# Kernel optimization log

Measured on AMD Instinct MI355X. Metric: run time of the kernel, lower is better.

The kernel has to match this reference:

```python
import jax, jax.numpy as jnp
import numpy as np

N_NODES = 50000
N_EDGES = 800000
D_IN = 128
D_OUT = 128
HEADS = 2
NEG_SLOPE = 0.2  # PyG GATConv default


def _gat_layer(x, src, dst, W, att_src, att_dst, bias):
    """One PyG-style GATConv with concat=False (mean over heads).
    x: [N, d_in], W: [d_in, H*d_out], att_src/att_dst: [H, d_out], bias: [d_out].
    Edge (j=src -> i=dst); softmax normalized over incoming edges of each dst node.
    """
    n = x.shape[0]
    d_out = att_src.shape[1]
    h = (x @ W).reshape(n, HEADS, d_out)                       # [N, H, D]
    a_s = jnp.einsum('nhd,hd->nh', h, att_src)                 # [N, H]
    a_d = jnp.einsum('nhd,hd->nh', h, att_dst)                 # [N, H]
    e = jax.nn.leaky_relu(a_s[src] + a_d[dst], NEG_SLOPE)      # [E, H]
    # numerically stable segment softmax over dst
    m = jax.ops.segment_max(e, dst, num_segments=n)            # [N, H]
    p = jnp.exp(e - m[dst])                                    # [E, H]
    s = jax.ops.segment_sum(p, dst, num_segments=n)            # [N, H]
    alpha = p / s[dst]                                         # [E, H]
    msg = h[src] * alpha[:, :, None]                           # [E, H, D]
    out = jax.ops.segment_sum(msg, dst, num_segments=n)        # [N, H, D]
    return out.mean(axis=1) + bias                             # concat=False -> mean heads


def setup_inputs() -> dict:
    key = jax.random.key(0)
    ks = jax.random.split(key, 10)
    sc = 0.05
    return {
        'x': jax.random.normal(ks[0], (N_NODES, D_IN), dtype=jnp.float32),
        'edge_index': jax.random.randint(ks[1], (2, N_EDGES), 0, N_NODES, dtype=jnp.int64),
        'W1': jax.random.normal(ks[2], (D_IN, HEADS * D_IN), dtype=jnp.float32) * sc,
        'att_src1': jax.random.normal(ks[3], (HEADS, D_IN), dtype=jnp.float32) * sc,
        'att_dst1': jax.random.normal(ks[4], (HEADS, D_IN), dtype=jnp.float32) * sc,
        'b1': jnp.zeros((D_IN,), dtype=jnp.float32),
        'W2': jax.random.normal(ks[5], (D_IN, HEADS * D_OUT), dtype=jnp.float32) * sc,
        'att_src2': jax.random.normal(ks[6], (HEADS, D_OUT), dtype=jnp.float32) * sc,
        'att_dst2': jax.random.normal(ks[7], (HEADS, D_OUT), dtype=jnp.float32) * sc,
        'b2': jnp.zeros((D_OUT,), dtype=jnp.float32),
    }


def reference(x, edge_index, W1, att_src1, att_dst1, b1, W2, att_src2, att_dst2, b2):
    n = x.shape[0]
    # PyG GATConv adds self-loops by default -> every node has >=1 incoming edge
    loops = jnp.arange(n, dtype=edge_index.dtype)
    src = jnp.concatenate([edge_index[0], loops])
    dst = jnp.concatenate([edge_index[1], loops])
    x = _gat_layer(x, src, dst, W1, att_src1, att_dst1, b1)
    x = _gat_layer(x, src, dst, W2, att_src2, att_dst2, b2)
    return x
```

## Files before the change

kernel.cpp:

```cpp
#include <hip/hip_runtime.h>
#include <hip/hip_bf16.h>

#define D 128
#define NCOLS 256
#define NPB 256
#define CAP 12288
#define P1CHUNK 4096

using f16x8 = __attribute__((ext_vector_type(8))) _Float16;
using f16x2 = __attribute__((ext_vector_type(2))) _Float16;
using f32x4 = __attribute__((ext_vector_type(4))) float;

__device__ inline int edge_val(const void* ei, int is32, long long idx) {
    if (is32) return ((const int*)ei)[idx];
    return (int)(((const long long*)ei)[idx]);
}

__global__ __launch_bounds__(256) void attprep_kernel(
    const float* __restrict__ W1, const float* __restrict__ as1,
    const float* __restrict__ ad1, float* __restrict__ v_s1,
    float* __restrict__ v_d1, _Float16* __restrict__ wT1,
    const float* __restrict__ W2, const float* __restrict__ as2,
    const float* __restrict__ ad2, float* __restrict__ v_s2,
    float* __restrict__ v_d2, _Float16* __restrict__ wT2,
    const void* __restrict__ ei, int* __restrict__ flag, int* __restrict__ gcnt) {
    int tid = threadIdx.x;
    if (blockIdx.x == 34) {
        gcnt[tid] = 0;
        if (tid == 0) *flag = 0;
        __syncthreads();
        const unsigned* u = (const unsigned*)ei;
        if (u[2 * tid + 1] != 0) *flag = 1;
        return;
    }
    int layer = blockIdx.x >= 17;
    int bx = blockIdx.x - (layer ? 17 : 0);
    const float* W = layer ? W2 : W1;
    const float* att_s = layer ? as2 : as1;
    const float* att_d = layer ? ad2 : ad1;
    float* v_s = layer ? v_s2 : v_s1;
    float* v_d = layer ? v_d2 : v_d1;
    _Float16* wT = layer ? wT2 : wT1;
    if (bx == 16) {
        int h = tid >> 7, d = tid & 127;
        const float* wrow = W + d * NCOLS + h * D;
        const float* as = att_s + h * D;
        const float* ad = att_d + h * D;
        float ss = 0.f, sd = 0.f;
        for (int i = 0; i < D; i += 4) {
            float4 wv = *reinterpret_cast<const float4*>(wrow + i);
            float4 av = *reinterpret_cast<const float4*>(as + i);
            float4 dv = *reinterpret_cast<const float4*>(ad + i);
            ss += wv.x * av.x + wv.y * av.y + wv.z * av.z + wv.w * av.w;
            sd += wv.x * dv.x + wv.y * dv.y + wv.z * dv.z + wv.w * dv.w;
        }
        v_s[tid] = ss;
        v_d[tid] = sd;
    } else {
        int base = bx * 2048 + tid * 8;
#pragma unroll
        for (int t = 0; t < 8; t += 4) {
            int f = base + t;
            int kk = f >> 7, i = f & 127;
            int h = kk >> 7, d = kk & 127;
            float4 wv = *reinterpret_cast<const float4*>(W + d * NCOLS + h * D + i);
            wT[(size_t)(i + 0) * NCOLS + kk] = (_Float16)(0.5f * wv.x);
            wT[(size_t)(i + 1) * NCOLS + kk] = (_Float16)(0.5f * wv.y);
            wT[(size_t)(i + 2) * NCOLS + kk] = (_Float16)(0.5f * wv.z);
            wT[(size_t)(i + 3) * NCOLS + kk] = (_Float16)(0.5f * wv.w);
        }
    }
}

__global__ __launch_bounds__(256) void binprep_kernel(
    const void* __restrict__ ei, const int* __restrict__ flag,
    unsigned* __restrict__ bins, int* __restrict__ gcnt, int E, int nbuck,
    const float* __restrict__ x, const float* __restrict__ v_s,
    const float* __restrict__ v_d, _Float16* __restrict__ xh,
    float* __restrict__ a_s, float* __restrict__ a_d, int n, int NBB) {
    __shared__ int cnt[256], cur[256], gb[256];
    int tid = threadIdx.x;
    if ((int)blockIdx.x < NBB) {
        int base = blockIdx.x * P1CHUNK;
        int m = min(P1CHUNK, E - base);
        int is32 = *flag;
        cnt[tid] = 0; cur[tid] = 0;
        __syncthreads();
        for (int i = tid; i < m; i += 256) {
            int dst = edge_val(ei, is32, (long long)E + base + i);
            atomicAdd(&cnt[dst >> 8], 1);
        }
        __syncthreads();
        if (tid < nbuck && cnt[tid] > 0) gb[tid] = atomicAdd(&gcnt[tid], cnt[tid]);
        else gb[tid] = 0;
        __syncthreads();
        for (int i = tid; i < m; i += 256) {
            int src = edge_val(ei, is32, base + i);
            int dst = edge_val(ei, is32, (long long)E + base + i);
            int b = dst >> 8;
            int pos = gb[b] + atomicAdd(&cur[b], 1);
            if (pos < CAP)
                bins[(size_t)b * CAP + pos] = ((unsigned)(dst & 255) << 16) | (unsigned)src;
        }
        return;
    }
    int lane = tid & 63;
    int node = ((int)blockIdx.x - NBB) * 4 + (tid >> 6);
    if (node >= n) return;
    float2 xv = *reinterpret_cast<const float2*>(x + (size_t)node * D + 2 * lane);
    f16x2 hx = {(_Float16)xv.x, (_Float16)xv.y};
    *reinterpret_cast<f16x2*>(xh + (size_t)node * D + 2 * lane) = hx;
    float2 vs0 = *reinterpret_cast<const float2*>(v_s + 2 * lane);
    float2 vs1 = *reinterpret_cast<const float2*>(v_s + D + 2 * lane);
    float2 vd0 = *reinterpret_cast<const float2*>(v_d + 2 * lane);
    float2 vd1 = *reinterpret_cast<const float2*>(v_d + D + 2 * lane);
    float s0 = xv.x * vs0.x + xv.y * vs0.y;
    float s1 = xv.x * vs1.x + xv.y * vs1.y;
    float d0 = xv.x * vd0.x + xv.y * vd0.y;
    float d1 = xv.x * vd1.x + xv.y * vd1.y;
#pragma unroll
    for (int off = 1; off < 64; off <<= 1) {
        s0 += __shfl_xor(s0, off, 64);
        s1 += __shfl_xor(s1, off, 64);
        d0 += __shfl_xor(d0, off, 64);
        d1 += __shfl_xor(d1, off, 64);
    }
    if (lane == 0) {
        *reinterpret_cast<float2*>(a_s + (size_t)node * 2) = make_float2(s0, s1);
        *reinterpret_cast<float2*>(a_d + (size_t)node * 2) = make_float2(d0, d1);
    }
}

__global__ __launch_bounds__(256) void build_kernel(
    const unsigned* __restrict__ bins, const int* __restrict__ gcnt,
    int* __restrict__ row_ptr, int* __restrict__ csr_src, int n, int nbuck) {
    __shared__ unsigned items[CAP];
    __shared__ int deg[256], sc[256], cur[256], pref[256];
    int b = blockIdx.x, tid = threadIdx.x;
    int node0 = b * NPB;
    int nn = min(n - node0, NPB);
    int cnt = min(gcnt[b], CAP);
    int t = 0;
    if (tid < b) {
        int lo = tid * NPB, hi = min(n, lo + NPB);
        t = min(gcnt[tid], CAP) + (hi - lo);
    }
    pref[tid] = t;
    const unsigned* src = bins + (size_t)b * CAP;
    for (int i = tid; i < cnt; i += 256) items[i] = src[i];
    deg[tid] = (tid < nn) ? 1 : 0;
    __syncthreads();
#pragma unroll
    for (int off = 128; off >= 1; off >>= 1) {
        if (tid < off) pref[tid] += pref[tid + off];
        __syncthreads();
    }
    int gb = pref[0];
    for (int i = tid; i < cnt; i += 256) atomicAdd(&deg[(items[i] >> 16) & 255], 1);
    __syncthreads();
    int d = deg[tid];
    sc[tid] = d;
    __syncthreads();
#pragma unroll
    for (int off = 1; off < 256; off <<= 1) {
        int u = (tid >= off) ? sc[tid - off] : 0;
        __syncthreads();
        sc[tid] += u;
        __syncthreads();
    }
    int incl = sc[tid];
    int excl = incl - d;
    if (tid < nn) row_ptr[node0 + tid + 1] = gb + incl;
    if (b == 0 && tid == 0) row_ptr[0] = 0;
    cur[tid] = excl + ((tid < nn) ? 1 : 0);
    if (tid < nn) csr_src[gb + excl] = node0 + tid;
    __syncthreads();
    for (int i = tid; i < cnt; i += 256) {
        unsigned it = items[i];
        int p = atomicAdd(&cur[(it >> 16) & 255], 1);
        csr_src[gb + p] = (int)(it & 0xFFFFu);
    }
}

__global__ __launch_bounds__(256) void agg_mfma_kernel(
    const _Float16* __restrict__ xh, const float* __restrict__ a_s,
    const float* __restrict__ a_d, const int* __restrict__ row_ptr,
    const int* __restrict__ csr_src, const _Float16* __restrict__ wT,
    const float* __restrict__ bias, const float* __restrict__ vs_next,
    const float* __restrict__ vd_next, float* __restrict__ as_next,
    float* __restrict__ ad_next, float* __restrict__ outf,
    _Float16* __restrict__ outh, int n) {
    __shared__ __align__(16) _Float16 Alds[8 * 512];
    __shared__ float part[4][16][4];
    int tid = threadIdx.x;
    int wave = tid >> 6, lane = tid & 63;
    int m0 = blockIdx.x * 16;
    int sub = lane >> 4, cq = lane & 15;

    const _Float16* xb = xh + 8 * cq;
    for (int nd = 0; nd < 4; ++nd) {
        int nl = wave * 4 + nd;
        int node = m0 + nl;
        if (node >= n) break;
        int beg = row_ptr[node], end = row_ptr[node + 1];
        float2 ad = *reinterpret_cast<const float2*>(a_d + (size_t)node * 2);
        float s0 = 0.f, s1 = 0.f;
        float acc0[8] = {}, acc1[8] = {};
        for (int chunk = beg; chunk < end; chunk += 64) {
            int cnt = min(64, end - chunk);
            int j_l = 0;
            unsigned pp_l = 0;
            if (lane < cnt) {
                j_l = csr_src[chunk + lane];
                float2 as2 = *reinterpret_cast<const float2*>(a_s + (size_t)j_l * 2);
                float e0 = as2.x + ad.x; e0 = (e0 > 0.f) ? e0 : 0.2f * e0;
                float e1 = as2.y + ad.y; e1 = (e1 > 0.f) ? e1 : 0.2f * e1;
                f16x2 pq = {(_Float16)__expf(e0), (_Float16)__expf(e1)};
                pp_l = __builtin_bit_cast(unsigned, pq);
                s0 += (float)pq[0];
                s1 += (float)pq[1];
            }
#pragma unroll 4
            for (int k = 0; k < cnt; k += 4) {
                int idx = k + sub;
                unsigned ppu = (unsigned)__shfl((int)pp_l, idx, 64);
                int j = __shfl(j_l, idx, 64);
                f16x2 pq = __builtin_bit_cast(f16x2, ppu);
                float p0 = (float)pq[0], p1 = (float)pq[1];
                f16x8 hv = *reinterpret_cast<const f16x8*>(xb + (size_t)j * D);
#pragma unroll
                for (int i = 0; i < 8; ++i) {
                    float h = (float)hv[i];
                    acc0[i] += p0 * h;
                    acc1[i] += p1 * h;
                }
            }
        }
#pragma unroll
        for (int i = 0; i < 8; ++i) {
            acc0[i] += __shfl_xor(acc0[i], 16, 64);
            acc0[i] += __shfl_xor(acc0[i], 32, 64);
            acc1[i] += __shfl_xor(acc1[i], 16, 64);
            acc1[i] += __shfl_xor(acc1[i], 32, 64);
        }
#pragma unroll
        for (int off = 1; off < 64; off <<= 1) {
            s0 += __shfl_xor(s0, off, 64);
            s1 += __shfl_xor(s1, off, 64);
        }
        if (sub == 0) {
            float i0 = 1.f / s0, i1 = 1.f / s1;
            f16x8 o0, o1;
#pragma unroll
            for (int i = 0; i < 8; ++i) {
                o0[i] = (_Float16)(acc0[i] * i0);
                o1[i] = (_Float16)(acc1[i] * i1);
            }
            int kt0 = cq >> 2, g0 = cq & 3;
            *reinterpret_cast<f16x8*>(Alds + kt0 * 512 + (g0 * 16 + nl) * 8)       = o0;
            *reinterpret_cast<f16x8*>(Alds + (4 + kt0) * 512 + (g0 * 16 + nl) * 8) = o1;
        }
    }
    __syncthreads();

    int ml = lane & 15, g = lane >> 4;
    f32x4 accA = {}, accB = {};
    int nt0 = wave * 2, nt1 = wave * 2 + 1;
    const _Float16* b0 = wT + (size_t)(nt0 * 16 + ml) * NCOLS + 8 * g;
    const _Float16* b1 = wT + (size_t)(nt1 * 16 + ml) * NCOLS + 8 * g;
#pragma unroll
    for (int kt = 0; kt < 8; ++kt) {
        f16x8 av = *reinterpret_cast<const f16x8*>(Alds + kt * 512 + lane * 8);
        int ko = kt * 32;
        f16x8 bv0 = *reinterpret_cast<const f16x8*>(b0 + ko);
        f16x8 bv1 = *reinterpret_cast<const f16x8*>(b1 + ko);
        accA = __builtin_amdgcn_mfma_f32_16x16x32_f16(av, bv0, accA, 0, 0, 0);
        accB = __builtin_amdgcn_mfma_f32_16x16x32_f16(av, bv1, accB, 0, 0, 0);
    }

    int col0 = nt0 * 16 + ml, col1 = nt1 * 16 + ml;
    float bA = bias[col0], bB = bias[col1];
    float vsA0 = 0.f, vsA1 = 0.f, vdA0 = 0.f, vdA1 = 0.f;
    float vsB0 = 0.f, vsB1 = 0.f, vdB0 = 0.f, vdB1 = 0.f;
    if (vs_next) {
        vsA0 = vs_next[col0]; vsA1 = vs_next[D + col0];
        vdA0 = vd_next[col0]; vdA1 = vd_next[D + col0];
        vsB0 = vs_next[col1]; vsB1 = vs_next[D + col1];
        vdB0 = vd_next[col1]; vdB1 = vd_next[D + col1];
    }

#pragma unroll
    for (int r = 0; r < 4; ++r) {
        int lrow = g * 4 + r;
        int orow = m0 + lrow;
        float vA = accA[r] + bA;
        float vB = accB[r] + bB;
        if (orow < n) {
            if (outf) {
                outf[(size_t)orow * D + col0] = vA;
                outf[(size_t)orow * D + col1] = vB;
            }
            if (outh) {
                outh[(size_t)orow * D + col0] = (_Float16)vA;
                outh[(size_t)orow * D + col1] = (_Float16)vB;
            }
        }
        if (vs_next) {
            float ps0 = vA * vsA0 + vB * vsB0;
            float ps1 = vA * vsA1 + vB * vsB1;
            float pd0 = vA * vdA0 + vB * vdB0;
            float pd1 = vA * vdA1 + vB * vdB1;
#pragma unroll
            for (int off = 1; off < 16; off <<= 1) {
                ps0 += __shfl_xor(ps0, off, 64);
                ps1 += __shfl_xor(ps1, off, 64);
                pd0 += __shfl_xor(pd0, off, 64);
                pd1 += __shfl_xor(pd1, off, 64);
            }
            if (ml == 0) {
                part[wave][lrow][0] = ps0;
                part[wave][lrow][1] = ps1;
                part[wave][lrow][2] = pd0;
                part[wave][lrow][3] = pd1;
            }
        }
    }
    if (vs_next) {
        __syncthreads();
        if (tid < 64) {
            int row = tid >> 2, q = tid & 3;
            int node = m0 + row;
            if (node < n) {
                float v = part[0][row][q] + part[1][row][q]
                        + part[2][row][q] + part[3][row][q];
                float* dstp = (q < 2) ? as_next : ad_next;
                dstp[(size_t)node * 2 + (q & 1)] = v;
            }
        }
    }
}

extern "C" void kernel_launch(void* const* d_in, const int* in_sizes, int n_in,
                              void* d_out, int out_size, void* d_ws, size_t ws_size,
                              hipStream_t stream) {
    const float* x    = (const float*)d_in[0];
    const void*  ei   = d_in[1];
    const float* W1   = (const float*)d_in[2];
    const float* as1v = (const float*)d_in[3];
    const float* ad1v = (const float*)d_in[4];
    const float* b1   = (const float*)d_in[5];
    const float* W2   = (const float*)d_in[6];
    const float* as2v = (const float*)d_in[7];
    const float* ad2v = (const float*)d_in[8];
    const float* b2   = (const float*)d_in[9];
    float* out = (float*)d_out;

    const int N  = in_sizes[0] / D;
    const int E  = in_sizes[1] / 2;
    const int ET = E + N;
    const int NBUCK = (N + NPB - 1) / NPB;
    const int NBB = (E + P1CHUNK - 1) / P1CHUNK;

    char* w = (char*)d_ws;
    size_t off = 0;
    auto alloc = [&](size_t bytes) {
        void* p = w + off;
        off = (off + bytes + 15) & ~(size_t)15;
        return p;
    };
    int*      flag    = (int*)     alloc(16);
    int*      gcnt    = (int*)     alloc(256 * 4);
    unsigned* bins    = (unsigned*)alloc((size_t)NBUCK * CAP * 4);
    int*      row_ptr = (int*)     alloc((size_t)(N + 1) * 4);
    int*      csr_src = (int*)     alloc((size_t)ET * 4);
    float*    v_s1    = (float*)   alloc(NCOLS * 4);
    float*    v_d1    = (float*)   alloc(NCOLS * 4);
    _Float16* wT1     = (_Float16*)alloc((size_t)NCOLS * D * 2);
    float*    v_s2    = (float*)   alloc(NCOLS * 4);
    float*    v_d2    = (float*)   alloc(NCOLS * 4);
    _Float16* wT2     = (_Float16*)alloc((size_t)NCOLS * D * 2);
    float*    a_s1    = (float*)   alloc((size_t)N * 2 * 4);
    float*    a_d1    = (float*)   alloc((size_t)N * 2 * 4);
    float*    a_s2    = (float*)   alloc((size_t)N * 2 * 4);
    float*    a_d2    = (float*)   alloc((size_t)N * 2 * 4);
    _Float16* xh      = (_Float16*)alloc((size_t)N * D * 2);
    _Float16* xmh     = (_Float16*)alloc((size_t)N * D * 2);

    hipLaunchKernelGGL(attprep_kernel, dim3(35), dim3(256), 0, stream,
                       W1, as1v, ad1v, v_s1, v_d1, wT1,
                       W2, as2v, ad2v, v_s2, v_d2, wT2, ei, flag, gcnt);
    hipLaunchKernelGGL(binprep_kernel, dim3(NBB + (N + 3) / 4), dim3(256), 0, stream,
                       ei, flag, bins, gcnt, E, NBUCK,
                       x, v_s1, v_d1, xh, a_s1, a_d1, N, NBB);
    hipLaunchKernelGGL(build_kernel, dim3(NBUCK), dim3(256), 0, stream,
                       bins, gcnt, row_ptr, csr_src, N, NBUCK);
    hipLaunchKernelGGL(agg_mfma_kernel, dim3((N + 15) / 16), dim3(256), 0, stream,
                       xh, a_s1, a_d1, row_ptr, csr_src, wT1, b1,
                       v_s2, v_d2, a_s2, a_d2, (float*)nullptr, xmh, N);
    hipLaunchKernelGGL(agg_mfma_kernel, dim3((N + 15) / 16), dim3(256), 0, stream,
                       xmh, a_s2, a_d2, row_ptr, csr_src, wT2, b2,
                       (const float*)nullptr, (const float*)nullptr,
                       (float*)nullptr, (float*)nullptr, out, (_Float16*)nullptr, N);
}
```

Measured before the change: 179.2 us.

## Assign one node per wave with 512-thread blocks and swizzle the LDS A tile

The aggregation kernel now runs 8 waves per block, and each wave gathers a single destination node instead of looping over 4 nodes in sequence. Each wave then computes one 16-column MFMA output tile over the block's 8 rows. This spreads the irregular gather across more independent waves, aiming for better latency hiding and load balance. An XOR swizzle on the LDS A-tile writes and reads is added to reduce bank conflicts. In exchange, half the rows of each 16-row MFMA tile are unused, and the weight tile is fetched by twice as many blocks.

```diff
diff --git a/kernel.cpp b/kernel.cpp
--- a/kernel.cpp
+++ b/kernel.cpp
@@ -182,7 +182,7 @@
     }
 }
 
-__global__ __launch_bounds__(256) void agg_mfma_kernel(
+__global__ __launch_bounds__(512) void agg_mfma_kernel(
     const _Float16* __restrict__ xh, const float* __restrict__ a_s,
     const float* __restrict__ a_d, const int* __restrict__ row_ptr,
     const int* __restrict__ csr_src, const _Float16* __restrict__ wT,
@@ -191,21 +191,19 @@
     float* __restrict__ ad_next, float* __restrict__ outf,
     _Float16* __restrict__ outh, int n) {
     __shared__ __align__(16) _Float16 Alds[8 * 512];
-    __shared__ float part[4][16][4];
+    __shared__ float part[8][8][4];
     int tid = threadIdx.x;
     int wave = tid >> 6, lane = tid & 63;
-    int m0 = blockIdx.x * 16;
+    int m0 = blockIdx.x * 8;
     int sub = lane >> 4, cq = lane & 15;
-
-    const _Float16* xb = xh + 8 * cq;
-    for (int nd = 0; nd < 4; ++nd) {
-        int nl = wave * 4 + nd;
-        int node = m0 + nl;
-        if (node >= n) break;
+    int node = m0 + wave;
+
+    if (node < n) {
         int beg = row_ptr[node], end = row_ptr[node + 1];
         float2 ad = *reinterpret_cast<const float2*>(a_d + (size_t)node * 2);
         float s0 = 0.f, s1 = 0.f;
         float acc0[8] = {}, acc1[8] = {};
+        const _Float16* xb = xh + 8 * cq;
         for (int chunk = beg; chunk < end; chunk += 64) {
             int cnt = min(64, end - chunk);
             int j_l = 0;
@@ -257,84 +255,75 @@
                 o1[i] = (_Float16)(acc1[i] * i1);
             }
             int kt0 = cq >> 2, g0 = cq & 3;
-            *reinterpret_cast<f16x8*>(Alds + kt0 * 512 + (g0 * 16 + nl) * 8)       = o0;
-            *reinterpret_cast<f16x8*>(Alds + (4 + kt0) * 512 + (g0 * 16 + nl) * 8) = o1;
+            int swz = ((kt0 & 3) << 3) ^ ((g0 & 1) << 5);
+            int e0i = (kt0 * 512 + (g0 * 16 + wave) * 8) ^ swz;
+            int e1i = ((kt0 + 4) * 512 + (g0 * 16 + wave) * 8) ^ swz;
+            *reinterpret_cast<f16x8*>(Alds + e0i) = o0;
+            *reinterpret_cast<f16x8*>(Alds + e1i) = o1;
         }
     }
     __syncthreads();
 
     int ml = lane & 15, g = lane >> 4;
-    f32x4 accA = {}, accB = {};
-    int nt0 = wave * 2, nt1 = wave * 2 + 1;
-    const _Float16* b0 = wT + (size_t)(nt0 * 16 + ml) * NCOLS + 8 * g;
-    const _Float16* b1 = wT + (size_t)(nt1 * 16 + ml) * NCOLS + 8 * g;
+    int nt = wave;
+    const _Float16* bB = wT + (size_t)(nt * 16 + ml) * NCOLS + 8 * g;
+    f32x4 acc = {};
 #pragma unroll
     for (int kt = 0; kt < 8; ++kt) {
-        f16x8 av = *reinterpret_cast<const f16x8*>(Alds + kt * 512 + lane * 8);
-        int ko = kt * 32;
-        f16x8 bv0 = *reinterpret_cast<const f16x8*>(b0 + ko);
-        f16x8 bv1 = *reinterpret_cast<const f16x8*>(b1 + ko);
-        accA = __builtin_amdgcn_mfma_f32_16x16x32_f16(av, bv0, accA, 0, 0, 0);
-        accB = __builtin_amdgcn_mfma_f32_16x16x32_f16(av, bv1, accB, 0, 0, 0);
-    }
-
-    int col0 = nt0 * 16 + ml, col1 = nt1 * 16 + ml;
-    float bA = bias[col0], bB = bias[col1];
-    float vsA0 = 0.f, vsA1 = 0.f, vdA0 = 0.f, vdA1 = 0.f;
-    float vsB0 = 0.f, vsB1 = 0.f, vdB0 = 0.f, vdB1 = 0.f;
+        int swzr = ((kt & 3) << 3) ^ ((g & 1) << 5);
+        f16x8 av = *reinterpret_cast<const f16x8*>(Alds + ((kt * 512 + lane * 8) ^ swzr));
+        f16x8 bv = *reinterpret_cast<const f16x8*>(bB + kt * 32);
+        acc = __builtin_amdgcn_mfma_f32_16x16x32_f16(av, bv, acc, 0, 0, 0);
+    }
+
+    int col = nt * 16 + ml;
+    float bC = bias[col];
+    float vs0 = 0.f, vs1 = 0.f, vd0 = 0.f, vd1 = 0.f;
     if (vs_next) {
-        vsA0 = vs_next[col0]; vsA1 = vs_next[D + col0];
-        vdA0 = vd_next[col0]; vdA1 = vd_next[D + col0];
-        vsB0 = vs_next[col1]; vsB1 = vs_next[D + col1];
-        vdB0 = vd_next[col1]; vdB1 = vd_next[D + col1];
+        vs0 = vs_next[col]; vs1 = vs_next[D + col];
+        vd0 = vd_next[col]; vd1 = vd_next[D + col];
     }
 
 #pragma unroll
     for (int r = 0; r < 4; ++r) {
         int lrow = g * 4 + r;
-        int orow = m0 + lrow;
-        float vA = accA[r] + bA;
-        float vB = accB[r] + bB;
-        if (orow < n) {
-            if (outf) {
-                outf[(size_t)orow * D + col0] = vA;
-                outf[(size_t)orow * D + col1] = vB;
-            }
-            if (outh) {
-                outh[(size_t)orow * D + col0] = (_Float16)vA;
-                outh[(size_t)orow * D + col1] = (_Float16)vB;
-            }
-        }
-        if (vs_next) {
-            float ps0 = vA * vsA0 + vB * vsB0;
-            float ps1 = vA * vsA1 + vB * vsB1;
-            float pd0 = vA * vdA0 + vB * vdB0;
-            float pd1 = vA * vdA1 + vB * vdB1;
-#pragma unroll
-            for (int off = 1; off < 16; off <<= 1) {
-                ps0 += __shfl_xor(ps0, off, 64);
-                ps1 += __shfl_xor(ps1, off, 64);
-                pd0 += __shfl_xor(pd0, off, 64);
-                pd1 += __shfl_xor(pd1, off, 64);
-            }
-            if (ml == 0) {
-                part[wave][lrow][0] = ps0;
-                part[wave][lrow][1] = ps1;
-                part[wave][lrow][2] = pd0;
-                part[wave][lrow][3] = pd1;
+        if (lrow < 8) {
+            int orow = m0 + lrow;
+            float v = acc[r] + bC;
+            if (orow < n) {
+                if (outf) outf[(size_t)orow * D + col] = v;
+                if (outh) outh[(size_t)orow * D + col] = (_Float16)v;
+            }
+            if (vs_next) {
+                float ps0 = v * vs0, ps1 = v * vs1;
+                float pd0 = v * vd0, pd1 = v * vd1;
+#pragma unroll
+                for (int off = 1; off < 16; off <<= 1) {
+                    ps0 += __shfl_xor(ps0, off, 64);
+                    ps1 += __shfl_xor(ps1, off, 64);
+                    pd0 += __shfl_xor(pd0, off, 64);
+                    pd1 += __shfl_xor(pd1, off, 64);
+                }
+                if (ml == 0) {
+                    part[wave][lrow][0] = ps0;
+                    part[wave][lrow][1] = ps1;
+                    part[wave][lrow][2] = pd0;
+                    part[wave][lrow][3] = pd1;
+                }
             }
         }
     }
     if (vs_next) {
         __syncthreads();
-        if (tid < 64) {
+        if (tid < 32) {
             int row = tid >> 2, q = tid & 3;
-            int node = m0 + row;
-            if (node < n) {
-                float v = part[0][row][q] + part[1][row][q]
-                        + part[2][row][q] + part[3][row][q];
+            int nd = m0 + row;
+            if (nd < n) {
+                float v = 0.f;
+#pragma unroll
+                for (int w8 = 0; w8 < 8; ++w8) v += part[w8][row][q];
                 float* dstp = (q < 2) ? as_next : ad_next;
-                dstp[(size_t)node * 2 + (q & 1)] = v;
+                dstp[(size_t)nd * 2 + (q & 1)] = v;
             }
         }
     }
@@ -394,10 +383,10 @@
                        x, v_s1, v_d1, xh, a_s1, a_d1, N, NBB);
     hipLaunchKernelGGL(build_kernel, dim3(NBUCK), dim3(256), 0, stream,
                        bins, gcnt, row_ptr, csr_src, N, NBUCK);
-    hipLaunchKernelGGL(agg_mfma_kernel, dim3((N + 15) / 16), dim3(256), 0, stream,
+    hipLaunchKernelGGL(agg_mfma_kernel, dim3((N + 7) / 8), dim3(512), 0, stream,
                        xh, a_s1, a_d1, row_ptr, csr_src, wT1, b1,
                        v_s2, v_d2, a_s2, a_d2, (float*)nullptr, xmh, N);
-    hipLaunchKernelGGL(agg_mfma_kernel, dim3((N + 15) / 16), dim3(256), 0, stream,
+    hipLaunchKernelGGL(agg_mfma_kernel, dim3((N + 7) / 8), dim3(512), 0, stream,
                        xmh, a_s2, a_d2, row_ptr, csr_src, wT2, b2,
                        (const float*)nullptr, (const float*)nullptr,
                        (float*)nullptr, (float*)nullptr, out, (_Float16*)nullptr, N);
```

Result: slower. 244.1 us (+36.2%).

## Sort nodes by in-degree to balance aggregation work across blocks

Applied to the files above, without the earlier changes.

Builds a per-node in-degree histogram during CSR construction, scans it, and produces a permutation that orders nodes by descending degree. The aggregation kernels then process nodes in that order, so each block's 16 nodes have similar edge counts, and results are scattered back to the original node indices. The goal is less wave imbalance and tail time from degree variance. The cost is two extra small kernel launches, global atomics, and scattered rather than contiguous output writes.

```diff
diff --git a/kernel.cpp b/kernel.cpp
--- a/kernel.cpp
+++ b/kernel.cpp
@@ -23,10 +23,12 @@
     const float* __restrict__ W2, const float* __restrict__ as2,
     const float* __restrict__ ad2, float* __restrict__ v_s2,
     float* __restrict__ v_d2, _Float16* __restrict__ wT2,
-    const void* __restrict__ ei, int* __restrict__ flag, int* __restrict__ gcnt) {
+    const void* __restrict__ ei, int* __restrict__ flag,
+    int* __restrict__ gcnt, int* __restrict__ ghist) {
     int tid = threadIdx.x;
     if (blockIdx.x == 34) {
         gcnt[tid] = 0;
+        ghist[tid] = 0;
         if (tid == 0) *flag = 0;
         __syncthreads();
         const unsigned* u = (const unsigned*)ei;
@@ -133,7 +135,8 @@
 
 __global__ __launch_bounds__(256) void build_kernel(
     const unsigned* __restrict__ bins, const int* __restrict__ gcnt,
-    int* __restrict__ row_ptr, int* __restrict__ csr_src, int n, int nbuck) {
+    int* __restrict__ row_ptr, int* __restrict__ csr_src,
+    int* __restrict__ ghist, int n, int nbuck) {
     __shared__ unsigned items[CAP];
     __shared__ int deg[256], sc[256], cur[256], pref[256];
     int b = blockIdx.x, tid = threadIdx.x;
@@ -159,6 +162,7 @@
     for (int i = tid; i < cnt; i += 256) atomicAdd(&deg[(items[i] >> 16) & 255], 1);
     __syncthreads();
     int d = deg[tid];
+    if (tid < nn) atomicAdd(&ghist[255 - min(d, 255)], 1);
     sc[tid] = d;
     __syncthreads();
 #pragma unroll
@@ -182,14 +186,53 @@
     }
 }
 
+__global__ void dscan_kernel(const int* __restrict__ ghist, int* __restrict__ gbase) {
+    __shared__ int a[256];
+    int tid = threadIdx.x;
+    a[tid] = ghist[tid];
+    __syncthreads();
+#pragma unroll
+    for (int off = 1; off < 256; off <<= 1) {
+        int u = (tid >= off) ? a[tid - off] : 0;
+        __syncthreads();
+        a[tid] += u;
+        __syncthreads();
+    }
+    gbase[tid] = a[tid] - ghist[tid];
+}
+
+__global__ __launch_bounds__(256) void perm_kernel(
+    const int* __restrict__ row_ptr, int* __restrict__ gbase,
+    int* __restrict__ perm, int n) {
+    __shared__ int cnt[256], gb[256], cur[256];
+    int tid = threadIdx.x;
+    int node0 = blockIdx.x * 256;
+    int nn = min(n - node0, 256);
+    cnt[tid] = 0; cur[tid] = 0;
+    __syncthreads();
+    int bin = 0;
+    if (tid < nn) {
+        int d = row_ptr[node0 + tid + 1] - row_ptr[node0 + tid];
+        bin = 255 - min(d, 255);
+        atomicAdd(&cnt[bin], 1);
+    }
+    __syncthreads();
+    gb[tid] = (cnt[tid] > 0) ? atomicAdd(&gbase[tid], cnt[tid]) : 0;
+    __syncthreads();
+    if (tid < nn) {
+        int p = gb[bin] + atomicAdd(&cur[bin], 1);
+        perm[p] = node0 + tid;
+    }
+}
+
 __global__ __launch_bounds__(256) void agg_mfma_kernel(
     const _Float16* __restrict__ xh, const float* __restrict__ a_s,
     const float* __restrict__ a_d, const int* __restrict__ row_ptr,
-    const int* __restrict__ csr_src, const _Float16* __restrict__ wT,
-    const float* __restrict__ bias, const float* __restrict__ vs_next,
-    const float* __restrict__ vd_next, float* __restrict__ as_next,
-    float* __restrict__ ad_next, float* __restrict__ outf,
-    _Float16* __restrict__ outh, int n) {
+    const int* __restrict__ csr_src, const int* __restrict__ perm,
+    const _Float16* __restrict__ wT, const float* __restrict__ bias,
+    const float* __restrict__ vs_next, const float* __restrict__ vd_next,
+    float* __restrict__ as_next, float* __restrict__ ad_next,
+    float* __restrict__ outf, _Float16* __restrict__ outh, int n) {
     __shared__ __align__(16) _Float16 Alds[8 * 512];
     __shared__ float part[4][16][4];
     int tid = threadIdx.x;
@@ -200,8 +243,9 @@
     const _Float16* xb = xh + 8 * cq;
     for (int nd = 0; nd < 4; ++nd) {
         int nl = wave * 4 + nd;
-        int node = m0 + nl;
-        if (node >= n) break;
+        int pidx = m0 + nl;
+        if (pidx >= n) break;
+        int node = perm[pidx];
         int beg = row_ptr[node], end = row_ptr[node + 1];
         float2 ad = *reinterpret_cast<const float2*>(a_d + (size_t)node * 2);
         float s0 = 0.f, s1 = 0.f;
@@ -292,17 +336,18 @@
 #pragma unroll
     for (int r = 0; r < 4; ++r) {
         int lrow = g * 4 + r;
-        int orow = m0 + lrow;
+        int pidx = m0 + lrow;
         float vA = accA[r] + bA;
         float vB = accB[r] + bB;
-        if (orow < n) {
+        if (pidx < n) {
+            int node = perm[pidx];
             if (outf) {
-                outf[(size_t)orow * D + col0] = vA;
-                outf[(size_t)orow * D + col1] = vB;
+                outf[(size_t)node * D + col0] = vA;
+                outf[(size_t)node * D + col1] = vB;
             }
             if (outh) {
-                outh[(size_t)orow * D + col0] = (_Float16)vA;
-                outh[(size_t)orow * D + col1] = (_Float16)vB;
+                outh[(size_t)node * D + col0] = (_Float16)vA;
+                outh[(size_t)node * D + col1] = (_Float16)vB;
             }
         }
         if (vs_next) {
@@ -329,8 +374,9 @@
         __syncthreads();
         if (tid < 64) {
             int row = tid >> 2, q = tid & 3;
-            int node = m0 + row;
-            if (node < n) {
+            int pidx = m0 + row;
+            if (pidx < n) {
+                int node = perm[pidx];
                 float v = part[0][row][q] + part[1][row][q]
                         + part[2][row][q] + part[3][row][q];
                 float* dstp = (q < 2) ? as_next : ad_next;
@@ -370,9 +416,12 @@
     };
     int*      flag    = (int*)     alloc(16);
     int*      gcnt    = (int*)     alloc(256 * 4);
+    int*      ghist   = (int*)     alloc(256 * 4);
+    int*      gbase   = (int*)     alloc(256 * 4);
     unsigned* bins    = (unsigned*)alloc((size_t)NBUCK * CAP * 4);
     int*      row_ptr = (int*)     alloc((size_t)(N + 1) * 4);
     int*      csr_src = (int*)     alloc((size_t)ET * 4);
+    int*      perm    = (int*)     alloc((size_t)N * 4);
     float*    v_s1    = (float*)   alloc(NCOLS * 4);
     float*    v_d1    = (float*)   alloc(NCOLS * 4);
     _Float16* wT1     = (_Float16*)alloc((size_t)NCOLS * D * 2);
@@ -388,17 +437,20 @@
 
     hipLaunchKernelGGL(attprep_kernel, dim3(35), dim3(256), 0, stream,
                        W1, as1v, ad1v, v_s1, v_d1, wT1,
-                       W2, as2v, ad2v, v_s2, v_d2, wT2, ei, flag, gcnt);
+                       W2, as2v, ad2v, v_s2, v_d2, wT2, ei, flag, gcnt, ghist);
     hipLaunchKernelGGL(binprep_kernel, dim3(NBB + (N + 3) / 4), dim3(256), 0, stream,
                        ei, flag, bins, gcnt, E, NBUCK,
                        x, v_s1, v_d1, xh, a_s1, a_d1, N, NBB);
     hipLaunchKernelGGL(build_kernel, dim3(NBUCK), dim3(256), 0, stream,
-                       bins, gcnt, row_ptr, csr_src, N, NBUCK);
+                       bins, gcnt, row_ptr, csr_src, ghist, N, NBUCK);
+    hipLaunchKernelGGL(dscan_kernel, dim3(1), dim3(256), 0, stream, ghist, gbase);
+    hipLaunchKernelGGL(perm_kernel, dim3(NBUCK), dim3(256), 0, stream,
+                       row_ptr, gbase, perm, N);
     hipLaunchKernelGGL(agg_mfma_kernel, dim3((N + 15) / 16), dim3(256), 0, stream,
-                       xh, a_s1, a_d1, row_ptr, csr_src, wT1, b1,
+                       xh, a_s1, a_d1, row_ptr, csr_src, perm, wT1, b1,
                        v_s2, v_d2, a_s2, a_d2, (float*)nullptr, xmh, N);
     hipLaunchKernelGGL(agg_mfma_kernel, dim3((N + 15) / 16), dim3(256), 0, stream,
-                       xmh, a_s2, a_d2, row_ptr, csr_src, wT2, b2,
+                       xmh, a_s2, a_d2, row_ptr, csr_src, perm, wT2, b2,
                        (const float*)nullptr, (const float*)nullptr,
                        (float*)nullptr, (float*)nullptr, out, (_Float16*)nullptr, N);
 }
```

Measured after the change: 336.9 us. 88.0% more time.
